# Optimization experiments

Hardware: AMD Instinct MI355X
Metric: run time of the kernel (lower is better)

Reference implementation:

```python
import jax, jax.numpy as jnp
import numpy as np

DIM = 256
HEADS = 8


def _ln(x, g, b, eps=1e-5):
    mu = jnp.mean(x, axis=-1, keepdims=True)
    var = jnp.var(x, axis=-1, keepdims=True)
    return (x - mu) * jax.lax.rsqrt(var + eps) * g + b


def setup_inputs() -> dict:
    key = jax.random.key(0)
    ks = jax.random.split(key, 12)
    d = DIM
    s = lambda fan: 1.0 / np.sqrt(fan)
    return {
        "x": jax.random.normal(ks[0], (1, d, 64, 64), dtype=jnp.float32),
        "ln1_g": jnp.ones((d,), jnp.float32),
        "ln1_b": jnp.zeros((d,), jnp.float32),
        "w_qkv": jax.random.normal(ks[1], (3 * d, d), jnp.float32) * s(d),
        "b_qkv": jnp.zeros((3 * d,), jnp.float32),
        "w_proj": jax.random.normal(ks[2], (d, d), jnp.float32) * s(d),
        "b_proj": jnp.zeros((d,), jnp.float32),
        "ln2_g": jnp.ones((d,), jnp.float32),
        "ln2_b": jnp.zeros((d,), jnp.float32),
        "w_mlp1": jax.random.normal(ks[3], (4 * d, d), jnp.float32) * s(d),
        "b_mlp1": jnp.zeros((4 * d,), jnp.float32),
        "w_mlp2": jax.random.normal(ks[4], (d, 4 * d), jnp.float32) * s(4 * d),
        "b_mlp2": jnp.zeros((d,), jnp.float32),
    }


def reference(x, ln1_g, ln1_b, w_qkv, b_qkv, w_proj, b_proj,
              ln2_g, ln2_b, w_mlp1, b_mlp1, w_mlp2, b_mlp2):
    B, C, H, W = x.shape
    hd = HEADS
    d = C // hd
    scale = d ** (-0.5)
    # work channels-last: [B, H, W, C] -> [B, HW, C]
    xl = jnp.transpose(x, (0, 2, 3, 1)).reshape(B, H * W, C)

    # --- attention branch ---
    xn = _ln(xl, ln1_g, ln1_b)
    qkv = jnp.einsum('bnc,oc->bno', xn, w_qkv) + b_qkv  # [B, N, 3C]
    q, k, v = jnp.split(qkv, 3, axis=-1)
    def heads(t):  # [B,N,C] -> [B,h,N,d]
        return jnp.transpose(t.reshape(B, H * W, hd, d), (0, 2, 1, 3))
    q, k, v = heads(q), heads(k), heads(v)
    attn = jax.nn.softmax(jnp.einsum('bhnd,bhmd->bhnm', q, k) * scale, axis=-1)
    out = jnp.einsum('bhnm,bhmd->bhnd', attn, v)  # [B,h,N,d]
    out = jnp.transpose(out, (0, 2, 1, 3)).reshape(B, H * W, C)
    xl = xl + jnp.einsum('bnc,oc->bno', out, w_proj) + b_proj

    # --- MLP branch ---
    xn = _ln(xl, ln2_g, ln2_b)
    h1 = jax.nn.gelu(jnp.einsum('bnc,oc->bno', xn, w_mlp1) + b_mlp1,
                     approximate=False)
    xl = xl + jnp.einsum('bnf,of->bno', h1, w_mlp2) + b_mlp2

    return jnp.transpose(xl.reshape(B, H, W, C), (0, 3, 1, 2))
```

## Files before the change

kernel.cpp:

```cpp
#include <hip/hip_runtime.h>
#include <hip/hip_bf16.h>

typedef __bf16 bf16_t;
typedef __bf16 bf16x8 __attribute__((ext_vector_type(8)));
typedef __bf16 bf16x4 __attribute__((ext_vector_type(4)));
typedef float  f32x4  __attribute__((ext_vector_type(4)));
typedef unsigned int uint;
typedef uint u32x4 __attribute__((ext_vector_type(4)));

#define MFMA(a,b,c) __builtin_amdgcn_mfma_f32_16x16x32_bf16((a),(b),(c),0,0,0)

__device__ __forceinline__ size_t pidx(int n, int k, int K) {
  return (size_t)(n >> 4) * (K << 4) + ((k >> 3) << 7) + ((n & 15) << 3) + (k & 7);
}

__device__ __forceinline__ uint packbf2(float lo, float hi) {
  unsigned short a = __builtin_bit_cast(unsigned short, (bf16_t)lo);
  unsigned short b = __builtin_bit_cast(unsigned short, (bf16_t)hi);
  return (uint)a | ((uint)b << 16);
}

__global__ __launch_bounds__(256) void prep(const float* __restrict__ w_qkv,
                                            const float* __restrict__ w_proj,
                                            const float* __restrict__ w_mlp1,
                                            const float* __restrict__ w_mlp2,
                                            bf16_t* __restrict__ wq, bf16_t* __restrict__ wp,
                                            bf16_t* __restrict__ w1, bf16_t* __restrict__ w2,
                                            const float* __restrict__ x,
                                            const float* __restrict__ g,
                                            const float* __restrict__ bta,
                                            float* __restrict__ xl,
                                            bf16_t* __restrict__ xn) {
  __shared__ float tile[256][33];
  __shared__ float psum[8][32], psq[8][32], mu_s[32], rs_s[32];
  int b = blockIdx.x;
  if (b < 384) {
    const float* src; bf16_t* dst; int t0, ksh;
    if (b < 96)       { src = w_qkv;  dst = wq; ksh = 5; t0 = b * 256; }
    else if (b < 128) { src = w_proj; dst = wp; ksh = 5; t0 = (b - 96) * 256; }
    else if (b < 256) { src = w_mlp1; dst = w1; ksh = 5; t0 = (b - 128) * 256; }
    else              { src = w_mlp2; dst = w2; ksh = 7; t0 = (b - 256) * 256; }
    int t = t0 + threadIdx.x;
    int n = t >> ksh, kb = t & ((1 << ksh) - 1);
    int K = 8 << ksh;
    const float* p = src + (size_t)n * K + kb * 8;
    float4 a = *(const float4*)p;
    float4 c = *(const float4*)(p + 4);
    bf16x8 o = {(bf16_t)a.x, (bf16_t)a.y, (bf16_t)a.z, (bf16_t)a.w,
                (bf16_t)c.x, (bf16_t)c.y, (bf16_t)c.z, (bf16_t)c.w};
    *(bf16x8*)(dst + (size_t)(n >> 4) * (K << 4) + kb * 128 + ((n & 15) << 3)) = o;
    return;
  }
  int t = threadIdx.x, n0 = (b - 384) * 32;
  int lane32 = t & 31, grp = t >> 5;
#pragma unroll
  for (int it = 0; it < 32; ++it) {
    int c = grp + it * 8;
    tile[c][lane32] = x[(size_t)c * 4096 + n0 + lane32];
  }
  __syncthreads();
  float s = 0.f, sq = 0.f;
#pragma unroll
  for (int ci = 0; ci < 32; ++ci) {
    float v = tile[grp * 32 + ci][lane32];
    s += v; sq += v * v;
  }
  psum[grp][lane32] = s; psq[grp][lane32] = sq;
  __syncthreads();
  if (t < 32) {
    float S = 0.f, Q = 0.f;
#pragma unroll
    for (int p = 0; p < 8; ++p) { S += psum[p][t]; Q += psq[p][t]; }
    float mu = S * (1.0f / 256.0f);
    float var = Q * (1.0f / 256.0f) - mu * mu;
    mu_s[t] = mu; rs_s[t] = rsqrtf(var + 1e-5f);
  }
  __syncthreads();
  {
    float mu = mu_s[lane32], rs = rs_s[lane32];
    int row = n0 + lane32;
    bf16_t* op = xn + (size_t)(row >> 4) * 4096 + ((row & 15) << 3);
#pragma unroll
    for (int cc8 = 0; cc8 < 4; ++cc8) {
      int c0 = grp * 32 + cc8 * 8;
      bf16x8 o;
#pragma unroll
      for (int j = 0; j < 8; ++j) {
        int c = c0 + j;
        o[j] = (bf16_t)((tile[c][lane32] - mu) * rs * g[c] + bta[c]);
      }
      *(bf16x8*)(op + ((c0 >> 3) << 7)) = o;
    }
  }
#pragma unroll
  for (int it = 0; it < 4; ++it) {
    int j = grp + it * 8;
#pragma unroll
    for (int c0 = 0; c0 < 256; c0 += 32)
      xl[(size_t)(n0 + j) * 256 + c0 + lane32] = tile[c0 + lane32][j];
  }
}

template <int K, int EPI, int RPW, int KS = 1>
__global__ __launch_bounds__(256) void gemm_bt(const bf16_t* __restrict__ A,
                                               const bf16_t* __restrict__ W,
                                               const float* __restrict__ bias,
                                               void* __restrict__ outp, int ldn) {
  constexpr int RB = RPW / 16;
  constexpr int KLEN = K / KS;
  int w = threadIdx.x >> 6, lane = threadIdx.x & 63;
  int quad = lane >> 4, idx = lane & 15;
  int row0 = blockIdx.x * (4 * RPW) + w * RPW;
  int col0 = blockIdx.y * 64;
  int kb0 = (KS > 1) ? blockIdx.z * KLEN : 0;
  f32x4 acc[RB][4];
#pragma unroll
  for (int rb = 0; rb < RB; ++rb)
#pragma unroll
    for (int nb = 0; nb < 4; ++nb) acc[rb][nb] = (f32x4){0.f, 0.f, 0.f, 0.f};
  const bf16_t* abase = A + (size_t)(row0 >> 4) * (K << 4) + quad * 128 + idx * 8;
  const bf16_t* wbase = W + (size_t)(col0 >> 4) * (K << 4) + quad * 128 + idx * 8;
#pragma unroll 4
  for (int k0 = kb0; k0 < kb0 + KLEN; k0 += 32) {
    bf16x8 a[RB];
#pragma unroll
    for (int rb = 0; rb < RB; ++rb)
      a[rb] = *(const bf16x8*)(abase + (size_t)rb * (K << 4) + k0 * 16);
#pragma unroll
    for (int nb = 0; nb < 4; ++nb) {
      bf16x8 b = *(const bf16x8*)(wbase + (size_t)nb * (K << 4) + k0 * 16);
#pragma unroll
      for (int rb = 0; rb < RB; ++rb) acc[rb][nb] = MFMA(a[rb], b, acc[rb][nb]);
    }
  }
#pragma unroll
  for (int nb = 0; nb < 4; ++nb) {
    int c = col0 + nb * 16 + idx;
    float bv = (EPI == 4) ? 0.f : bias[c];
#pragma unroll
    for (int rb = 0; rb < RB; ++rb)
#pragma unroll
      for (int r = 0; r < 4; ++r) {
        int rr = row0 + rb * 16 + quad * 4 + r;
        float v = acc[rb][nb][r] + bv;
        if constexpr (EPI == 1) {
          float z = v * (0.7978845608f + 0.0356774081f * v * v);
          float t = __builtin_amdgcn_exp2f(z * 2.885390082f);
          float th = 1.f - 2.f * __builtin_amdgcn_rcpf(t + 1.f);
          v = 0.5f * v * (1.f + th);
          ((bf16_t*)outp)[pidx(rr, c, ldn)] = (bf16_t)v;
        } else if constexpr (EPI == 4) {
          ((float*)outp)[((size_t)blockIdx.z * 4096 + rr) * ldn + c] = v;
        } else {
          bf16_t* qh = (bf16_t*)outp;
          bf16_t* kh = qh + 1048576;
          bf16_t* vp = kh + 1048576;
          if (c < 256) {
            qh[(size_t)(c >> 5) * 131072 + rr * 32 + (c & 31)] = (bf16_t)v;
          } else if (c < 512) {
            kh[(size_t)((c - 256) >> 5) * 131072 + rr * 32 + (c & 31)] = (bf16_t)v;
          } else {
            vp[(size_t)((c - 512) >> 5) * 131072 + (rr >> 5) * 1024 + (c & 31) * 32 + (rr & 31)] = (bf16_t)v;
          }
        }
      }
  }
}

#define SPLIT 4
__device__ __forceinline__ void quad_transpose(const uint p[4][2], bf16x8& lo, bf16x8& hi) {
  auto sA0 = __builtin_amdgcn_permlane32_swap((int)p[0][0], (int)p[1][0], false, false);
  auto sA1 = __builtin_amdgcn_permlane32_swap((int)p[0][1], (int)p[1][1], false, false);
  auto sB0 = __builtin_amdgcn_permlane16_swap(sA0[0], sA0[1], false, false);
  auto sB1 = __builtin_amdgcn_permlane16_swap(sA1[0], sA1[1], false, false);
  u32x4 w0 = {(uint)sB0[0], (uint)sB1[0], (uint)sB0[1], (uint)sB1[1]};
  lo = __builtin_bit_cast(bf16x8, w0);
  auto tA0 = __builtin_amdgcn_permlane32_swap((int)p[2][0], (int)p[3][0], false, false);
  auto tA1 = __builtin_amdgcn_permlane32_swap((int)p[2][1], (int)p[3][1], false, false);
  auto tB0 = __builtin_amdgcn_permlane16_swap(tA0[0], tA0[1], false, false);
  auto tB1 = __builtin_amdgcn_permlane16_swap(tA1[0], tA1[1], false, false);
  u32x4 w1 = {(uint)tB0[0], (uint)tB1[0], (uint)tB0[1], (uint)tB1[1]};
  hi = __builtin_bit_cast(bf16x8, w1);
}

__global__ __launch_bounds__(256, 4) void attn_split(const bf16_t* __restrict__ qkvh,
                                                     uint* __restrict__ o_part,
                                                     float* __restrict__ l_part) {
  int w = threadIdx.x >> 6, lane = threadIdx.x & 63;
  int quad = lane >> 4, idx = lane & 15;
  int h  = blockIdx.x & 7;
  int qt = (blockIdx.x >> 3) & 31;
  int sp = blockIdx.x >> 8;
  int qrow = qt * 128 + w * 32;
  const bf16_t* qh = qkvh + (size_t)h * 131072;
  const bf16_t* kh = qh + 8 * 131072;
  const bf16_t* vp = kh + 8 * 131072;
  const float cs = 0.25503518f;
  bf16x8 qr0 = *(const bf16x8*)(qh + (size_t)(qrow + idx) * 32 + quad * 8);
  bf16x8 qr1 = *(const bf16x8*)(qh + (size_t)(qrow + 16 + idx) * 32 + quad * 8);
  bf16x8 qf0, qf1;
#pragma unroll
  for (int j = 0; j < 8; ++j) {
    qf0[j] = (bf16_t)((float)qr0[j] * cs);
    qf1[j] = (bf16_t)((float)qr1[j] * cs);
  }
  float ls0 = 0.f, ls1 = 0.f;
  f32x4 o00 = {0.f,0.f,0.f,0.f}, o01 = {0.f,0.f,0.f,0.f};
  f32x4 o10 = {0.f,0.f,0.f,0.f}, o11 = {0.f,0.f,0.f,0.f};
  const f32x4 zero = {0.f,0.f,0.f,0.f};
  int kbase = sp * 1024;

  bf16x8 kf[4];
#pragma unroll
  for (int kb = 0; kb < 4; ++kb)
    kf[kb] = *(const bf16x8*)(kh + (size_t)(kbase + kb * 16 + idx) * 32 + quad * 8);

  for (int kt = 0; kt < 16; ++kt) {
    int k0 = kbase + kt * 64;
    int k1 = kbase + ((kt + 1) & 15) * 64;
    const bf16_t* vt = vp + (size_t)(k0 >> 5) * 1024 + quad * 8;
    bf16x8 vv0 = *(const bf16x8*)(vt + idx * 32);
    bf16x8 vv1 = *(const bf16x8*)(vt + (idx + 16) * 32);
    bf16x8 vv2 = *(const bf16x8*)(vt + 1024 + idx * 32);
    bf16x8 vv3 = *(const bf16x8*)(vt + 1024 + (idx + 16) * 32);
    bf16x8 kfn[4];
#pragma unroll
    for (int kb = 0; kb < 4; ++kb)
      kfn[kb] = *(const bf16x8*)(kh + (size_t)(k1 + kb * 16 + idx) * 32 + quad * 8);
    uint p0[4][2], p1[4][2];
#pragma unroll
    for (int kb = 0; kb < 4; ++kb) {
      f32x4 s0 = MFMA(kf[kb], qf0, zero);
      f32x4 s1 = MFMA(kf[kb], qf1, zero);
      float a0 = __builtin_amdgcn_exp2f(s0[0]), a1 = __builtin_amdgcn_exp2f(s0[1]);
      float a2 = __builtin_amdgcn_exp2f(s0[2]), a3 = __builtin_amdgcn_exp2f(s0[3]);
      float b0 = __builtin_amdgcn_exp2f(s1[0]), b1 = __builtin_amdgcn_exp2f(s1[1]);
      float b2 = __builtin_amdgcn_exp2f(s1[2]), b3 = __builtin_amdgcn_exp2f(s1[3]);
      ls0 += (a0 + a1) + (a2 + a3);
      ls1 += (b0 + b1) + (b2 + b3);
      p0[kb][0] = packbf2(a0, a1); p0[kb][1] = packbf2(a2, a3);
      p1[kb][0] = packbf2(b0, b1); p1[kb][1] = packbf2(b2, b3);
    }
    bf16x8 pa0, pa1, pb0, pb1;
    quad_transpose(p0, pa0, pa1);
    quad_transpose(p1, pb0, pb1);
    o00 = MFMA(pa0, vv0, o00);
    o01 = MFMA(pa0, vv1, o01);
    o10 = MFMA(pb0, vv0, o10);
    o11 = MFMA(pb0, vv1, o11);
    o00 = MFMA(pa1, vv2, o00);
    o01 = MFMA(pa1, vv3, o01);
    o10 = MFMA(pb1, vv2, o10);
    o11 = MFMA(pb1, vv3, o11);
#pragma unroll
    for (int kb = 0; kb < 4; ++kb) kf[kb] = kfn[kb];
  }
  ls0 += __shfl_xor(ls0, 16); ls0 += __shfl_xor(ls0, 32);
  ls1 += __shfl_xor(ls1, 16); ls1 += __shfl_xor(ls1, 32);
  if (quad == 0) {
    l_part[((size_t)sp * 8 + h) * 4096 + qrow + idx]      = ls0;
    l_part[((size_t)sp * 8 + h) * 4096 + qrow + 16 + idx] = ls1;
  }
#pragma unroll
  for (int r = 0; r < 4; ++r) {
    int n0 = qrow + quad * 4 + r;
    o_part[(((size_t)sp * 4096 + n0) * 8 + h) * 16 + idx] = packbf2(o00[r], o01[r]);
    int n1 = n0 + 16;
    o_part[(((size_t)sp * 4096 + n1) * 8 + h) * 16 + idx] = packbf2(o10[r], o11[r]);
  }
}

__global__ __launch_bounds__(256) void attn_norm(const uint* __restrict__ o_part,
                                                 const float* __restrict__ l_part,
                                                 bf16_t* __restrict__ attn) {
  int t = blockIdx.x * 256 + threadIdx.x;
  int j0 = (t & 3) * 4;
  int h  = (t >> 2) & 7;
  int n  = t >> 5;
  float l = 0.f;
#pragma unroll
  for (int s = 0; s < SPLIT; ++s) l += l_part[((size_t)s * 8 + h) * 4096 + n];
  float inv = 1.0f / l;
  float alo[4] = {0.f,0.f,0.f,0.f}, ahi[4] = {0.f,0.f,0.f,0.f};
#pragma unroll
  for (int s = 0; s < SPLIT; ++s) {
    const uint* p = o_part + (((size_t)s * 4096 + n) * 8 + h) * 16 + j0;
    uint4 v = *(const uint4*)p;
    uint vv[4] = {v.x, v.y, v.z, v.w};
#pragma unroll
    for (int jj = 0; jj < 4; ++jj) {
      alo[jj] += __builtin_bit_cast(float, vv[jj] << 16);
      ahi[jj] += __builtin_bit_cast(float, vv[jj] & 0xffff0000u);
    }
  }
  bf16x4 lo = {(bf16_t)(alo[0] * inv), (bf16_t)(alo[1] * inv),
               (bf16_t)(alo[2] * inv), (bf16_t)(alo[3] * inv)};
  bf16x4 hi = {(bf16_t)(ahi[0] * inv), (bf16_t)(ahi[1] * inv),
               (bf16_t)(ahi[2] * inv), (bf16_t)(ahi[3] * inv)};
  int k1 = h * 32 + j0;
  int k2 = k1 + 16;
  *(bf16x4*)(attn + (size_t)(n >> 4) * 4096 + ((k1 >> 3) << 7) + ((n & 15) << 3) + (k1 & 7)) = lo;
  *(bf16x4*)(attn + (size_t)(n >> 4) * 4096 + ((k2 >> 3) << 7) + ((n & 15) << 3) + (k2 & 7)) = hi;
}

__global__ __launch_bounds__(256) void combine_ln(const float* __restrict__ pp,
                                                  const float* __restrict__ xl,
                                                  const float* __restrict__ bias,
                                                  const float* __restrict__ g,
                                                  const float* __restrict__ bta,
                                                  float* __restrict__ xl2,
                                                  bf16_t* __restrict__ xn2) {
  int row  = blockIdx.x * 4 + (threadIdx.x >> 6);
  int lane = threadIdx.x & 63;
  size_t ri = (size_t)row * 64 + lane;
  float4 rr = ((const float4*)xl)[ri];
  float4 bb = ((const float4*)bias)[lane];
  float4 v = {rr.x + bb.x, rr.y + bb.y, rr.z + bb.z, rr.w + bb.w};
#pragma unroll
  for (int s = 0; s < 2; ++s) {
    float4 p = ((const float4*)pp)[ri + (size_t)s * 4096 * 64];
    v.x += p.x; v.y += p.y; v.z += p.z; v.w += p.w;
  }
  ((float4*)xl2)[ri] = v;
  float s  = v.x + v.y + v.z + v.w;
  float sq = v.x * v.x + v.y * v.y + v.z * v.z + v.w * v.w;
#pragma unroll
  for (int off = 32; off; off >>= 1) {
    s  += __shfl_xor(s, off);
    sq += __shfl_xor(sq, off);
  }
  float mu  = s * (1.0f / 256.0f);
  float var = sq * (1.0f / 256.0f) - mu * mu;
  float rs  = rsqrtf(var + 1e-5f);
  float4 gg = ((const float4*)g)[lane];
  float4 b2 = ((const float4*)bta)[lane];
  bf16x4 o = {(bf16_t)((v.x - mu) * rs * gg.x + b2.x),
              (bf16_t)((v.y - mu) * rs * gg.y + b2.y),
              (bf16_t)((v.z - mu) * rs * gg.z + b2.z),
              (bf16_t)((v.w - mu) * rs * gg.w + b2.w)};
  int k = lane * 4;
  *(bf16x4*)(xn2 + (size_t)(row >> 4) * 4096 + ((k >> 3) << 7) + ((row & 15) << 3) + (k & 7)) = o;
}

__global__ __launch_bounds__(256) void combine_transpose(const float* __restrict__ mp,
                                                         const float* __restrict__ xl2,
                                                         const float* __restrict__ bias,
                                                         float* __restrict__ dst) {
  __shared__ float tile[32][33];
  int n0 = blockIdx.x * 32, c0 = blockIdx.y * 32;
  int a = threadIdx.x & 31, b = threadIdx.x >> 5;
  float bv = bias[c0 + a];
#pragma unroll
  for (int i = 0; i < 4; ++i) {
    int n = b + i * 8;
    size_t base = (size_t)(n0 + n) * 256 + c0 + a;
    float v = xl2[base] + bv;
#pragma unroll
    for (int s = 0; s < 4; ++s) v += mp[(size_t)s * 1048576 + base];
    tile[a][n] = v;
  }
  __syncthreads();
#pragma unroll
  for (int i = 0; i < 4; ++i) {
    int c = b + i * 8;
    dst[(size_t)(c0 + c) * 4096 + n0 + a] = tile[c][a];
  }
}

extern "C" void kernel_launch(void* const* d_in, const int* in_sizes, int n_in,
                              void* d_out, int out_size, void* d_ws, size_t ws_size,
                              hipStream_t stream) {
  const float* x      = (const float*)d_in[0];
  const float* ln1_g  = (const float*)d_in[1];
  const float* ln1_b  = (const float*)d_in[2];
  const float* w_qkv  = (const float*)d_in[3];
  const float* b_qkv  = (const float*)d_in[4];
  const float* w_proj = (const float*)d_in[5];
  const float* b_proj = (const float*)d_in[6];
  const float* ln2_g  = (const float*)d_in[7];
  const float* ln2_b  = (const float*)d_in[8];
  const float* w_mlp1 = (const float*)d_in[9];
  const float* b_mlp1 = (const float*)d_in[10];
  const float* w_mlp2 = (const float*)d_in[11];
  const float* b_mlp2 = (const float*)d_in[12];

  char* ws = (char*)d_ws;
  bf16_t* qkvh   = (bf16_t*)(ws + 0);
  float*  xl     = (float*)(ws + (6u << 20));
  bf16_t* xn     = (bf16_t*)(ws + (10u << 20));
  uint*   o_part = (uint*)(ws + (12u << 20));
  bf16_t* attn   = (bf16_t*)(ws + (20u << 20));
  float*  pp     = (float*)(ws + (24u << 20));
  float*  xl2    = (float*)(ws + (10u << 20));
  bf16_t* xn2    = (bf16_t*)(ws + (14u << 20));
  bf16_t* h1     = (bf16_t*)(ws + 0);
  float*  mp     = (float*)(ws + (16u << 20));
  bf16_t* wq     = (bf16_t*)(ws + (32u << 20));
  bf16_t* wp     = wq + 196608;
  bf16_t* w1     = wp + 65536;
  bf16_t* w2     = w1 + 262144;
  float*  l_part = (float*)(ws + (34304u << 10));

  prep<<<512, 256, 0, stream>>>(w_qkv, w_proj, w_mlp1, w_mlp2, wq, wp, w1, w2,
                                x, ln1_g, ln1_b, xl, xn);

  gemm_bt<256, 3, 16><<<dim3(64, 12), 256, 0, stream>>>(xn, wq, b_qkv, qkvh, 768);
  attn_split<<<256 * SPLIT, 256, 0, stream>>>(qkvh, o_part, l_part);
  attn_norm<<<512, 256, 0, stream>>>(o_part, l_part, attn);

  gemm_bt<256, 4, 16, 2><<<dim3(64, 4, 2), 256, 0, stream>>>(attn, wp, nullptr, pp, 256);
  combine_ln<<<1024, 256, 0, stream>>>(pp, xl, b_proj, ln2_g, ln2_b, xl2, xn2);

  gemm_bt<256, 1, 16><<<dim3(64, 16), 256, 0, stream>>>(xn2, w1, b_mlp1, h1, 1024);
  gemm_bt<1024, 4, 16, 4><<<dim3(64, 4, 4), 256, 0, stream>>>(h1, w2, nullptr, mp, 256);
  combine_transpose<<<dim3(128, 8), 256, 0, stream>>>(mp, xl2, b_mlp2, (float*)d_out);
}
```

Before: 168.4 us.

## Fuse all stages into one persistent megakernel with atomic grid barriers

Turns each stage into a device function and runs all nine stages inside a single persistent kernel of 1024 blocks, with software grid barriers (atomic counter plus spin) between stages. This removes the per-launch overhead and the idle gaps between nine dependent kernel launches. In exchange, every block now waits at each barrier, the fused kernel needs enough registers and shared memory for the worst stage at occupancy 4, and a memset of the barrier counters is added. The code falls back to separate launches if occupancy is too low, and it relies on all 1024 blocks being resident at once to avoid deadlock.

```diff
diff --git a/kernel.cpp b/kernel.cpp
--- a/kernel.cpp
+++ b/kernel.cpp
@@ -9,6 +9,8 @@
 typedef uint u32x4 __attribute__((ext_vector_type(4)));
 
 #define MFMA(a,b,c) __builtin_amdgcn_mfma_f32_16x16x32_bf16((a),(b),(c),0,0,0)
+#define SPLIT 4
+#define NBLK 1024u
 
 __device__ __forceinline__ size_t pidx(int n, int k, int K) {
   return (size_t)(n >> 4) * (K << 4) + ((k >> 3) << 7) + ((n & 15) << 3) + (k & 7);
@@ -20,20 +22,30 @@
   return (uint)a | ((uint)b << 16);
 }
 
-__global__ __launch_bounds__(256) void prep(const float* __restrict__ w_qkv,
-                                            const float* __restrict__ w_proj,
-                                            const float* __restrict__ w_mlp1,
-                                            const float* __restrict__ w_mlp2,
-                                            bf16_t* __restrict__ wq, bf16_t* __restrict__ wp,
-                                            bf16_t* __restrict__ w1, bf16_t* __restrict__ w2,
-                                            const float* __restrict__ x,
-                                            const float* __restrict__ g,
-                                            const float* __restrict__ bta,
-                                            float* __restrict__ xl,
-                                            bf16_t* __restrict__ xn) {
-  __shared__ float tile[256][33];
-  __shared__ float psum[8][32], psq[8][32], mu_s[32], rs_s[32];
-  int b = blockIdx.x;
+struct PrepSM {
+  float tile[256][33];
+  float psum[8][32], psq[8][32], mu_s[32], rs_s[32];
+};
+struct CtrSM { float tile[32][33]; };
+
+__device__ __forceinline__ void gridbar(uint* bar, int slot) {
+  __threadfence();
+  __syncthreads();
+  if (threadIdx.x == 0) {
+    __hip_atomic_fetch_add(bar + slot * 32, 1u, __ATOMIC_ACQ_REL, __HIP_MEMORY_SCOPE_AGENT);
+    while (__hip_atomic_load(bar + slot * 32, __ATOMIC_ACQUIRE, __HIP_MEMORY_SCOPE_AGENT) < NBLK)
+      __builtin_amdgcn_s_sleep(1);
+  }
+  __syncthreads();
+  __threadfence();
+}
+
+__device__ __forceinline__ void prep_body(int b, char* sm,
+                                          const float* w_qkv, const float* w_proj,
+                                          const float* w_mlp1, const float* w_mlp2,
+                                          bf16_t* wq, bf16_t* wp, bf16_t* w1, bf16_t* w2,
+                                          const float* x, const float* g, const float* bta,
+                                          float* xl, bf16_t* xn) {
   if (b < 384) {
     const float* src; bf16_t* dst; int t0, ksh;
     if (b < 96)       { src = w_qkv;  dst = wq; ksh = 5; t0 = b * 256; }
@@ -51,33 +63,34 @@
     *(bf16x8*)(dst + (size_t)(n >> 4) * (K << 4) + kb * 128 + ((n & 15) << 3)) = o;
     return;
   }
+  PrepSM& S = *(PrepSM*)sm;
   int t = threadIdx.x, n0 = (b - 384) * 32;
   int lane32 = t & 31, grp = t >> 5;
 #pragma unroll
   for (int it = 0; it < 32; ++it) {
     int c = grp + it * 8;
-    tile[c][lane32] = x[(size_t)c * 4096 + n0 + lane32];
+    S.tile[c][lane32] = x[(size_t)c * 4096 + n0 + lane32];
   }
   __syncthreads();
   float s = 0.f, sq = 0.f;
 #pragma unroll
   for (int ci = 0; ci < 32; ++ci) {
-    float v = tile[grp * 32 + ci][lane32];
+    float v = S.tile[grp * 32 + ci][lane32];
     s += v; sq += v * v;
   }
-  psum[grp][lane32] = s; psq[grp][lane32] = sq;
+  S.psum[grp][lane32] = s; S.psq[grp][lane32] = sq;
   __syncthreads();
   if (t < 32) {
-    float S = 0.f, Q = 0.f;
-#pragma unroll
-    for (int p = 0; p < 8; ++p) { S += psum[p][t]; Q += psq[p][t]; }
-    float mu = S * (1.0f / 256.0f);
+    float Su = 0.f, Q = 0.f;
+#pragma unroll
+    for (int p = 0; p < 8; ++p) { Su += S.psum[p][t]; Q += S.psq[p][t]; }
+    float mu = Su * (1.0f / 256.0f);
     float var = Q * (1.0f / 256.0f) - mu * mu;
-    mu_s[t] = mu; rs_s[t] = rsqrtf(var + 1e-5f);
+    S.mu_s[t] = mu; S.rs_s[t] = rsqrtf(var + 1e-5f);
   }
   __syncthreads();
   {
-    float mu = mu_s[lane32], rs = rs_s[lane32];
+    float mu = S.mu_s[lane32], rs = S.rs_s[lane32];
     int row = n0 + lane32;
     bf16_t* op = xn + (size_t)(row >> 4) * 4096 + ((row & 15) << 3);
 #pragma unroll
@@ -87,7 +100,7 @@
 #pragma unroll
       for (int j = 0; j < 8; ++j) {
         int c = c0 + j;
-        o[j] = (bf16_t)((tile[c][lane32] - mu) * rs * g[c] + bta[c]);
+        o[j] = (bf16_t)((S.tile[c][lane32] - mu) * rs * g[c] + bta[c]);
       }
       *(bf16x8*)(op + ((c0 >> 3) << 7)) = o;
     }
@@ -97,22 +110,21 @@
     int j = grp + it * 8;
 #pragma unroll
     for (int c0 = 0; c0 < 256; c0 += 32)
-      xl[(size_t)(n0 + j) * 256 + c0 + lane32] = tile[c0 + lane32][j];
-  }
-}
-
-template <int K, int EPI, int RPW, int KS = 1>
-__global__ __launch_bounds__(256) void gemm_bt(const bf16_t* __restrict__ A,
-                                               const bf16_t* __restrict__ W,
-                                               const float* __restrict__ bias,
-                                               void* __restrict__ outp, int ldn) {
+      xl[(size_t)(n0 + j) * 256 + c0 + lane32] = S.tile[c0 + lane32][j];
+  }
+}
+
+template <int K, int EPI, int RPW, int KS>
+__device__ __forceinline__ void gemm_body(int bx, int by, int bz,
+                                          const bf16_t* A, const bf16_t* W,
+                                          const float* bias, void* outp, int ldn) {
   constexpr int RB = RPW / 16;
   constexpr int KLEN = K / KS;
   int w = threadIdx.x >> 6, lane = threadIdx.x & 63;
   int quad = lane >> 4, idx = lane & 15;
-  int row0 = blockIdx.x * (4 * RPW) + w * RPW;
-  int col0 = blockIdx.y * 64;
-  int kb0 = (KS > 1) ? blockIdx.z * KLEN : 0;
+  int row0 = bx * (4 * RPW) + w * RPW;
+  int col0 = by * 64;
+  int kb0 = (KS > 1) ? bz * KLEN : 0;
   f32x4 acc[RB][4];
 #pragma unroll
   for (int rb = 0; rb < RB; ++rb)
@@ -150,7 +162,7 @@
           v = 0.5f * v * (1.f + th);
           ((bf16_t*)outp)[pidx(rr, c, ldn)] = (bf16_t)v;
         } else if constexpr (EPI == 4) {
-          ((float*)outp)[((size_t)blockIdx.z * 4096 + rr) * ldn + c] = v;
+          ((float*)outp)[((size_t)bz * 4096 + rr) * ldn + c] = v;
         } else {
           bf16_t* qh = (bf16_t*)outp;
           bf16_t* kh = qh + 1048576;
@@ -167,7 +179,6 @@
   }
 }
 
-#define SPLIT 4
 __device__ __forceinline__ void quad_transpose(const uint p[4][2], bf16x8& lo, bf16x8& hi) {
   auto sA0 = __builtin_amdgcn_permlane32_swap((int)p[0][0], (int)p[1][0], false, false);
   auto sA1 = __builtin_amdgcn_permlane32_swap((int)p[0][1], (int)p[1][1], false, false);
@@ -183,14 +194,13 @@
   hi = __builtin_bit_cast(bf16x8, w1);
 }
 
-__global__ __launch_bounds__(256, 4) void attn_split(const bf16_t* __restrict__ qkvh,
-                                                     uint* __restrict__ o_part,
-                                                     float* __restrict__ l_part) {
+__device__ __forceinline__ void attn_body(int bid, const bf16_t* qkvh,
+                                          uint* o_part, float* l_part) {
   int w = threadIdx.x >> 6, lane = threadIdx.x & 63;
   int quad = lane >> 4, idx = lane & 15;
-  int h  = blockIdx.x & 7;
-  int qt = (blockIdx.x >> 3) & 31;
-  int sp = blockIdx.x >> 8;
+  int h  = bid & 7;
+  int qt = (bid >> 3) & 31;
+  int sp = bid >> 8;
   int qrow = qt * 128 + w * 32;
   const bf16_t* qh = qkvh + (size_t)h * 131072;
   const bf16_t* kh = qh + 8 * 131072;
@@ -270,10 +280,9 @@
   }
 }
 
-__global__ __launch_bounds__(256) void attn_norm(const uint* __restrict__ o_part,
-                                                 const float* __restrict__ l_part,
-                                                 bf16_t* __restrict__ attn) {
-  int t = blockIdx.x * 256 + threadIdx.x;
+__device__ __forceinline__ void attn_norm_body(int bid, const uint* o_part,
+                                               const float* l_part, bf16_t* attn) {
+  int t = bid * 256 + threadIdx.x;
   int j0 = (t & 3) * 4;
   int h  = (t >> 2) & 7;
   int n  = t >> 5;
@@ -303,14 +312,10 @@
   *(bf16x4*)(attn + (size_t)(n >> 4) * 4096 + ((k2 >> 3) << 7) + ((n & 15) << 3) + (k2 & 7)) = hi;
 }
 
-__global__ __launch_bounds__(256) void combine_ln(const float* __restrict__ pp,
-                                                  const float* __restrict__ xl,
-                                                  const float* __restrict__ bias,
-                                                  const float* __restrict__ g,
-                                                  const float* __restrict__ bta,
-                                                  float* __restrict__ xl2,
-                                                  bf16_t* __restrict__ xn2) {
-  int row  = blockIdx.x * 4 + (threadIdx.x >> 6);
+__device__ __forceinline__ void combine_ln_body(int bid, const float* pp, const float* xl,
+                                                const float* bias, const float* g,
+                                                const float* bta, float* xl2, bf16_t* xn2) {
+  int row  = bid * 4 + (threadIdx.x >> 6);
   int lane = threadIdx.x & 63;
   size_t ri = (size_t)row * 64 + lane;
   float4 rr = ((const float4*)xl)[ri];
@@ -342,12 +347,11 @@
   *(bf16x4*)(xn2 + (size_t)(row >> 4) * 4096 + ((k >> 3) << 7) + ((row & 15) << 3) + (k & 7)) = o;
 }
 
-__global__ __launch_bounds__(256) void combine_transpose(const float* __restrict__ mp,
-                                                         const float* __restrict__ xl2,
-                                                         const float* __restrict__ bias,
-                                                         float* __restrict__ dst) {
-  __shared__ float tile[32][33];
-  int n0 = blockIdx.x * 32, c0 = blockIdx.y * 32;
+__device__ __forceinline__ void combine_transpose_body(int bx, int by, char* sm,
+                                                       const float* mp, const float* xl2,
+                                                       const float* bias, float* dst) {
+  CtrSM& S = *(CtrSM*)sm;
+  int n0 = bx * 32, c0 = by * 32;
   int a = threadIdx.x & 31, b = threadIdx.x >> 5;
   float bv = bias[c0 + a];
 #pragma unroll
@@ -357,14 +361,96 @@
     float v = xl2[base] + bv;
 #pragma unroll
     for (int s = 0; s < 4; ++s) v += mp[(size_t)s * 1048576 + base];
-    tile[a][n] = v;
+    S.tile[a][n] = v;
   }
   __syncthreads();
 #pragma unroll
   for (int i = 0; i < 4; ++i) {
     int c = b + i * 8;
-    dst[(size_t)(c0 + c) * 4096 + n0 + a] = tile[c][a];
-  }
+    dst[(size_t)(c0 + c) * 4096 + n0 + a] = S.tile[c][a];
+  }
+}
+
+__global__ __launch_bounds__(256, 4) void mega(const float* x,
+                                               const float* ln1_g, const float* ln1_b,
+                                               const float* w_qkv, const float* b_qkv,
+                                               const float* w_proj, const float* b_proj,
+                                               const float* ln2_g, const float* ln2_b,
+                                               const float* w_mlp1, const float* b_mlp1,
+                                               const float* w_mlp2, const float* b_mlp2,
+                                               float* out, char* ws) {
+  __shared__ __align__(16) char sm[sizeof(PrepSM)];
+  int bid = blockIdx.x;
+
+  bf16_t* qkvh   = (bf16_t*)(ws + 0);
+  float*  xl     = (float*)(ws + (6u << 20));
+  bf16_t* xn     = (bf16_t*)(ws + (10u << 20));
+  uint*   o_part = (uint*)(ws + (12u << 20));
+  bf16_t* attn   = (bf16_t*)(ws + (20u << 20));
+  float*  pp     = (float*)(ws + (24u << 20));
+  float*  xl2    = (float*)(ws + (10u << 20));
+  bf16_t* xn2    = (bf16_t*)(ws + (14u << 20));
+  bf16_t* h1     = (bf16_t*)(ws + 0);
+  float*  mp     = (float*)(ws + (16u << 20));
+  bf16_t* wq     = (bf16_t*)(ws + (32u << 20));
+  bf16_t* wp     = wq + 196608;
+  bf16_t* w1     = wp + 65536;
+  bf16_t* w2     = w1 + 262144;
+  float*  l_part = (float*)(ws + (34304u << 10));
+  uint*   bar    = (uint*)(ws + (34u << 20));
+
+  if (bid < 512)
+    prep_body(bid, sm, w_qkv, w_proj, w_mlp1, w_mlp2, wq, wp, w1, w2,
+              x, ln1_g, ln1_b, xl, xn);
+  gridbar(bar, 0);
+  if (bid < 768)
+    gemm_body<256, 3, 16, 1>(bid & 63, bid >> 6, 0, xn, wq, b_qkv, qkvh, 768);
+  gridbar(bar, 1);
+  attn_body(bid, qkvh, o_part, l_part);
+  gridbar(bar, 2);
+  if (bid < 512)
+    attn_norm_body(bid, o_part, l_part, attn);
+  gridbar(bar, 3);
+  if (bid < 512)
+    gemm_body<256, 4, 16, 2>(bid & 63, (bid >> 6) & 3, bid >> 8, attn, wp, nullptr, pp, 256);
+  gridbar(bar, 4);
+  combine_ln_body(bid, pp, xl, b_proj, ln2_g, ln2_b, xl2, xn2);
+  gridbar(bar, 5);
+  gemm_body<256, 1, 16, 1>(bid & 63, bid >> 6, 0, xn2, w1, b_mlp1, h1, 1024);
+  gridbar(bar, 6);
+  gemm_body<1024, 4, 16, 4>(bid & 63, (bid >> 6) & 3, bid >> 8, h1, w2, nullptr, mp, 256);
+  gridbar(bar, 7);
+  combine_transpose_body(bid & 127, bid >> 7, sm, mp, xl2, b_mlp2, out);
+}
+
+__global__ __launch_bounds__(256) void prep_k(const float* w_qkv, const float* w_proj,
+                                              const float* w_mlp1, const float* w_mlp2,
+                                              bf16_t* wq, bf16_t* wp, bf16_t* w1, bf16_t* w2,
+                                              const float* x, const float* g,
+                                              const float* bta, float* xl, bf16_t* xn) {
+  __shared__ __align__(16) char sm[sizeof(PrepSM)];
+  prep_body(blockIdx.x, sm, w_qkv, w_proj, w_mlp1, w_mlp2, wq, wp, w1, w2, x, g, bta, xl, xn);
+}
+template <int K, int EPI, int RPW, int KS = 1>
+__global__ __launch_bounds__(256) void gemm_k(const bf16_t* A, const bf16_t* W,
+                                              const float* bias, void* outp, int ldn) {
+  gemm_body<K, EPI, RPW, KS>(blockIdx.x, blockIdx.y, blockIdx.z, A, W, bias, outp, ldn);
+}
+__global__ __launch_bounds__(256, 4) void attn_k(const bf16_t* qkvh, uint* o_part, float* l_part) {
+  attn_body(blockIdx.x, qkvh, o_part, l_part);
+}
+__global__ __launch_bounds__(256) void attn_norm_k(const uint* o_part, const float* l_part, bf16_t* attn) {
+  attn_norm_body(blockIdx.x, o_part, l_part, attn);
+}
+__global__ __launch_bounds__(256) void combine_ln_k(const float* pp, const float* xl,
+                                                    const float* bias, const float* g,
+                                                    const float* bta, float* xl2, bf16_t* xn2) {
+  combine_ln_body(blockIdx.x, pp, xl, bias, g, bta, xl2, xn2);
+}
+__global__ __launch_bounds__(256) void combine_transpose_k(const float* mp, const float* xl2,
+                                                           const float* bias, float* dst) {
+  __shared__ __align__(16) char sm[sizeof(CtrSM)];
+  combine_transpose_body(blockIdx.x, blockIdx.y, sm, mp, xl2, bias, dst);
 }
 
 extern "C" void kernel_launch(void* const* d_in, const int* in_sizes, int n_in,
@@ -383,8 +469,9 @@
   const float* b_mlp1 = (const float*)d_in[10];
   const float* w_mlp2 = (const float*)d_in[11];
   const float* b_mlp2 = (const float*)d_in[12];
-
+  float* out = (float*)d_out;
   char* ws = (char*)d_ws;
+
   bf16_t* qkvh   = (bf16_t*)(ws + 0);
   float*  xl     = (float*)(ws + (6u << 20));
   bf16_t* xn     = (bf16_t*)(ws + (10u << 20));
@@ -400,18 +487,31 @@
   bf16_t* w1     = wp + 65536;
   bf16_t* w2     = w1 + 262144;
   float*  l_part = (float*)(ws + (34304u << 10));
-
-  prep<<<512, 256, 0, stream>>>(w_qkv, w_proj, w_mlp1, w_mlp2, wq, wp, w1, w2,
-                                x, ln1_g, ln1_b, xl, xn);
-
-  gemm_bt<256, 3, 16><<<dim3(64, 12), 256, 0, stream>>>(xn, wq, b_qkv, qkvh, 768);
-  attn_split<<<256 * SPLIT, 256, 0, stream>>>(qkvh, o_part, l_part);
-  attn_norm<<<512, 256, 0, stream>>>(o_part, l_part, attn);
-
-  gemm_bt<256, 4, 16, 2><<<dim3(64, 4, 2), 256, 0, stream>>>(attn, wp, nullptr, pp, 256);
-  combine_ln<<<1024, 256, 0, stream>>>(pp, xl, b_proj, ln2_g, ln2_b, xl2, xn2);
-
-  gemm_bt<256, 1, 16><<<dim3(64, 16), 256, 0, stream>>>(xn2, w1, b_mlp1, h1, 1024);
-  gemm_bt<1024, 4, 16, 4><<<dim3(64, 4, 4), 256, 0, stream>>>(h1, w2, nullptr, mp, 256);
-  combine_transpose<<<dim3(128, 8), 256, 0, stream>>>(mp, xl2, b_mlp2, (float*)d_out);
-}
+  uint*   bar    = (uint*)(ws + (34u << 20));
+
+  static int mega_ok = -1;
+  if (mega_ok < 0) {
+    int nb = 0;
+    hipError_t e = hipOccupancyMaxActiveBlocksPerMultiprocessor(&nb, mega, 256, 0);
+    mega_ok = (e == hipSuccess && nb >= 4) ? 1 : 0;
+  }
+
+  if (mega_ok) {
+    hipMemsetAsync(bar, 0, 4096, stream);
+    mega<<<NBLK, 256, 0, stream>>>(x, ln1_g, ln1_b, w_qkv, b_qkv, w_proj, b_proj,
+                                   ln2_g, ln2_b, w_mlp1, b_mlp1, w_mlp2, b_mlp2,
+                                   out, ws);
+    return;
+  }
+
+  prep_k<<<512, 256, 0, stream>>>(w_qkv, w_proj, w_mlp1, w_mlp2, wq, wp, w1, w2,
+                                  x, ln1_g, ln1_b, xl, xn);
+  gemm_k<256, 3, 16><<<dim3(64, 12), 256, 0, stream>>>(xn, wq, b_qkv, qkvh, 768);
+  attn_k<<<256 * SPLIT, 256, 0, stream>>>(qkvh, o_part, l_part);
+  attn_norm_k<<<512, 256, 0, stream>>>(o_part, l_part, attn);
+  gemm_k<256, 4, 16, 2><<<dim3(64, 4, 2), 256, 0, stream>>>(attn, wp, nullptr, pp, 256);
+  combine_ln_k<<<1024, 256, 0, stream>>>(pp, xl, b_proj, ln2_g, ln2_b, xl2, xn2);
+  gemm_k<256, 1, 16><<<dim3(64, 16), 256, 0, stream>>>(xn2, w1, b_mlp1, h1, 1024);
+  gemm_k<1024, 4, 16, 4><<<dim3(64, 4, 4), 256, 0, stream>>>(h1, w2, nullptr, mp, 256);
+  combine_transpose_k<<<dim3(128, 8), 256, 0, stream>>>(mp, xl2, b_mlp2, (float*)d_out);
+}
```

Result: no change. 169.3 us (+0.5%).

## Halve query rows per wave in split attention to double occupancy

Applied to the files above, without the earlier changes.

Each attention wave now handles 16 query rows instead of 32, so twice as many blocks are launched and launch bounds ask for 8 blocks per CU. The software prefetch of the next K tile is dropped and K is loaded inline. The aim is to cut register pressure and raise occupancy so more waves hide latency. In exchange, each K/V tile is reused across fewer query rows, which doubles K/V load traffic, and K loads are no longer overlapped with the previous tile's compute.

```diff
diff --git a/kernel.cpp b/kernel.cpp
--- a/kernel.cpp
+++ b/kernel.cpp
@@ -9,6 +9,7 @@
 typedef uint u32x4 __attribute__((ext_vector_type(4)));
 
 #define MFMA(a,b,c) __builtin_amdgcn_mfma_f32_16x16x32_bf16((a),(b),(c),0,0,0)
+#define SPLIT 4
 
 __device__ __forceinline__ size_t pidx(int n, int k, int K) {
   return (size_t)(n >> 4) * (K << 4) + ((k >> 3) << 7) + ((n & 15) << 3) + (k & 7);
@@ -167,7 +168,6 @@
   }
 }
 
-#define SPLIT 4
 __device__ __forceinline__ void quad_transpose(const uint p[4][2], bf16x8& lo, bf16x8& hi) {
   auto sA0 = __builtin_amdgcn_permlane32_swap((int)p[0][0], (int)p[1][0], false, false);
   auto sA1 = __builtin_amdgcn_permlane32_swap((int)p[0][1], (int)p[1][1], false, false);
@@ -183,90 +183,59 @@
   hi = __builtin_bit_cast(bf16x8, w1);
 }
 
-__global__ __launch_bounds__(256, 4) void attn_split(const bf16_t* __restrict__ qkvh,
+__global__ __launch_bounds__(256, 8) void attn_split(const bf16_t* __restrict__ qkvh,
                                                      uint* __restrict__ o_part,
                                                      float* __restrict__ l_part) {
   int w = threadIdx.x >> 6, lane = threadIdx.x & 63;
   int quad = lane >> 4, idx = lane & 15;
   int h  = blockIdx.x & 7;
-  int qt = (blockIdx.x >> 3) & 31;
-  int sp = blockIdx.x >> 8;
-  int qrow = qt * 128 + w * 32;
+  int qt = (blockIdx.x >> 3) & 63;
+  int sp = blockIdx.x >> 9;
+  int qrow = qt * 64 + w * 16;
   const bf16_t* qh = qkvh + (size_t)h * 131072;
   const bf16_t* kh = qh + 8 * 131072;
   const bf16_t* vp = kh + 8 * 131072;
   const float cs = 0.25503518f;
   bf16x8 qr0 = *(const bf16x8*)(qh + (size_t)(qrow + idx) * 32 + quad * 8);
-  bf16x8 qr1 = *(const bf16x8*)(qh + (size_t)(qrow + 16 + idx) * 32 + quad * 8);
-  bf16x8 qf0, qf1;
-#pragma unroll
-  for (int j = 0; j < 8; ++j) {
-    qf0[j] = (bf16_t)((float)qr0[j] * cs);
-    qf1[j] = (bf16_t)((float)qr1[j] * cs);
-  }
-  float ls0 = 0.f, ls1 = 0.f;
+  bf16x8 qf0;
+#pragma unroll
+  for (int j = 0; j < 8; ++j) qf0[j] = (bf16_t)((float)qr0[j] * cs);
+  float ls0 = 0.f;
   f32x4 o00 = {0.f,0.f,0.f,0.f}, o01 = {0.f,0.f,0.f,0.f};
-  f32x4 o10 = {0.f,0.f,0.f,0.f}, o11 = {0.f,0.f,0.f,0.f};
   const f32x4 zero = {0.f,0.f,0.f,0.f};
   int kbase = sp * 1024;
 
-  bf16x8 kf[4];
-#pragma unroll
-  for (int kb = 0; kb < 4; ++kb)
-    kf[kb] = *(const bf16x8*)(kh + (size_t)(kbase + kb * 16 + idx) * 32 + quad * 8);
-
   for (int kt = 0; kt < 16; ++kt) {
     int k0 = kbase + kt * 64;
-    int k1 = kbase + ((kt + 1) & 15) * 64;
     const bf16_t* vt = vp + (size_t)(k0 >> 5) * 1024 + quad * 8;
     bf16x8 vv0 = *(const bf16x8*)(vt + idx * 32);
     bf16x8 vv1 = *(const bf16x8*)(vt + (idx + 16) * 32);
     bf16x8 vv2 = *(const bf16x8*)(vt + 1024 + idx * 32);
     bf16x8 vv3 = *(const bf16x8*)(vt + 1024 + (idx + 16) * 32);
-    bf16x8 kfn[4];
-#pragma unroll
-    for (int kb = 0; kb < 4; ++kb)
-      kfn[kb] = *(const bf16x8*)(kh + (size_t)(k1 + kb * 16 + idx) * 32 + quad * 8);
-    uint p0[4][2], p1[4][2];
+    uint p0[4][2];
 #pragma unroll
     for (int kb = 0; kb < 4; ++kb) {
-      f32x4 s0 = MFMA(kf[kb], qf0, zero);
-      f32x4 s1 = MFMA(kf[kb], qf1, zero);
+      bf16x8 kf = *(const bf16x8*)(kh + (size_t)(k0 + kb * 16 + idx) * 32 + quad * 8);
+      f32x4 s0 = MFMA(kf, qf0, zero);
       float a0 = __builtin_amdgcn_exp2f(s0[0]), a1 = __builtin_amdgcn_exp2f(s0[1]);
       float a2 = __builtin_amdgcn_exp2f(s0[2]), a3 = __builtin_amdgcn_exp2f(s0[3]);
-      float b0 = __builtin_amdgcn_exp2f(s1[0]), b1 = __builtin_amdgcn_exp2f(s1[1]);
-      float b2 = __builtin_amdgcn_exp2f(s1[2]), b3 = __builtin_amdgcn_exp2f(s1[3]);
       ls0 += (a0 + a1) + (a2 + a3);
-      ls1 += (b0 + b1) + (b2 + b3);
       p0[kb][0] = packbf2(a0, a1); p0[kb][1] = packbf2(a2, a3);
-      p1[kb][0] = packbf2(b0, b1); p1[kb][1] = packbf2(b2, b3);
     }
-    bf16x8 pa0, pa1, pb0, pb1;
+    bf16x8 pa0, pa1;
     quad_transpose(p0, pa0, pa1);
-    quad_transpose(p1, pb0, pb1);
     o00 = MFMA(pa0, vv0, o00);
     o01 = MFMA(pa0, vv1, o01);
-    o10 = MFMA(pb0, vv0, o10);
-    o11 = MFMA(pb0, vv1, o11);
     o00 = MFMA(pa1, vv2, o00);
     o01 = MFMA(pa1, vv3, o01);
-    o10 = MFMA(pb1, vv2, o10);
-    o11 = MFMA(pb1, vv3, o11);
-#pragma unroll
-    for (int kb = 0; kb < 4; ++kb) kf[kb] = kfn[kb];
   }
   ls0 += __shfl_xor(ls0, 16); ls0 += __shfl_xor(ls0, 32);
-  ls1 += __shfl_xor(ls1, 16); ls1 += __shfl_xor(ls1, 32);
-  if (quad == 0) {
-    l_part[((size_t)sp * 8 + h) * 4096 + qrow + idx]      = ls0;
-    l_part[((size_t)sp * 8 + h) * 4096 + qrow + 16 + idx] = ls1;
-  }
+  if (quad == 0)
+    l_part[((size_t)sp * 8 + h) * 4096 + qrow + idx] = ls0;
 #pragma unroll
   for (int r = 0; r < 4; ++r) {
     int n0 = qrow + quad * 4 + r;
     o_part[(((size_t)sp * 4096 + n0) * 8 + h) * 16 + idx] = packbf2(o00[r], o01[r]);
-    int n1 = n0 + 16;
-    o_part[(((size_t)sp * 4096 + n1) * 8 + h) * 16 + idx] = packbf2(o10[r], o11[r]);
   }
 }
 
@@ -405,7 +374,7 @@
                                 x, ln1_g, ln1_b, xl, xn);
 
   gemm_bt<256, 3, 16><<<dim3(64, 12), 256, 0, stream>>>(xn, wq, b_qkv, qkvh, 768);
-  attn_split<<<256 * SPLIT, 256, 0, stream>>>(qkvh, o_part, l_part);
+  attn_split<<<512 * SPLIT, 256, 0, stream>>>(qkvh, o_part, l_part);
   attn_norm<<<512, 256, 0, stream>>>(o_part, l_part, attn);
 
   gemm_bt<256, 4, 16, 2><<<dim3(64, 4, 2), 256, 0, stream>>>(attn, wp, nullptr, pp, 256);
```

Measured after the change: 193.2 us. 14.8% more time.

## Fold reduction epilogues into producer kernels via last-arrival atomic counters

Applied to the files above, without the earlier changes.

Removes the separate attn_norm, combine_ln and combine_transpose launches. The last block of each group to finish, detected with an atomic ticket counter, performs the split-K or split-KV reduction plus the following elementwise work. This saves three kernel launches and their inter-kernel gaps. In exchange it adds a memset, threadfences and atomics, and the tail work now runs serially in a few last blocks, which may leave the GPU underutilized at the end of each kernel.

```diff
diff --git a/kernel.cpp b/kernel.cpp
--- a/kernel.cpp
+++ b/kernel.cpp
@@ -9,6 +9,7 @@
 typedef uint u32x4 __attribute__((ext_vector_type(4)));
 
 #define MFMA(a,b,c) __builtin_amdgcn_mfma_f32_16x16x32_bf16((a),(b),(c),0,0,0)
+#define SPLIT 4
 
 __device__ __forceinline__ size_t pidx(int n, int k, int K) {
   return (size_t)(n >> 4) * (K << 4) + ((k >> 3) << 7) + ((n & 15) << 3) + (k & 7);
@@ -18,6 +19,20 @@
   unsigned short a = __builtin_bit_cast(unsigned short, (bf16_t)lo);
   unsigned short b = __builtin_bit_cast(unsigned short, (bf16_t)hi);
   return (uint)a | ((uint)b << 16);
+}
+
+__device__ __forceinline__ bool last_arrival(uint* tk, int grp, uint members) {
+  __syncthreads();
+  __threadfence();
+  __shared__ uint oldv;
+  __syncthreads();
+  if (threadIdx.x == 0)
+    oldv = __hip_atomic_fetch_add(tk + grp, 1u, __ATOMIC_ACQ_REL,
+                                  __HIP_MEMORY_SCOPE_AGENT);
+  __syncthreads();
+  bool last = (oldv == members - 1);
+  if (last) __threadfence();
+  return last;
 }
 
 __global__ __launch_bounds__(256) void prep(const float* __restrict__ w_qkv,
@@ -101,11 +116,18 @@
   }
 }
 
-template <int K, int EPI, int RPW, int KS = 1>
+template <int K, int EPI, int RPW, int KS = 1, int FOLD = 0>
 __global__ __launch_bounds__(256) void gemm_bt(const bf16_t* __restrict__ A,
                                                const bf16_t* __restrict__ W,
                                                const float* __restrict__ bias,
-                                               void* __restrict__ outp, int ldn) {
+                                               void* __restrict__ outp, int ldn,
+                                               uint* __restrict__ tk,
+                                               const float* __restrict__ f0,
+                                               const float* __restrict__ f1,
+                                               const float* __restrict__ f2,
+                                               const float* __restrict__ f3,
+                                               float* __restrict__ f4,
+                                               void* __restrict__ f5) {
   constexpr int RB = RPW / 16;
   constexpr int KLEN = K / KS;
   int w = threadIdx.x >> 6, lane = threadIdx.x & 63;
@@ -165,9 +187,82 @@
         }
       }
   }
-}
-
-#define SPLIT 4
+
+  if constexpr (FOLD == 1) {
+    if (last_arrival(tk, blockIdx.x, 8)) {
+      int t = threadIdx.x;
+      int ln = t & 63;
+      const float* pp = (const float*)outp;
+#pragma unroll 2
+      for (int rr = 0; rr < 16; ++rr) {
+        int row = blockIdx.x * 64 + rr * 4 + (t >> 6);
+        size_t ri = (size_t)row * 64 + ln;
+        float4 r4 = ((const float4*)f0)[ri];
+        float4 bb = ((const float4*)f1)[ln];
+        float4 v = {r4.x + bb.x, r4.y + bb.y, r4.z + bb.z, r4.w + bb.w};
+#pragma unroll
+        for (int s = 0; s < 2; ++s) {
+          float4 p = ((const float4*)pp)[ri + (size_t)s * 4096 * 64];
+          v.x += p.x; v.y += p.y; v.z += p.z; v.w += p.w;
+        }
+        ((float4*)f4)[ri] = v;
+        float s  = v.x + v.y + v.z + v.w;
+        float sq = v.x * v.x + v.y * v.y + v.z * v.z + v.w * v.w;
+#pragma unroll
+        for (int off = 32; off; off >>= 1) {
+          s  += __shfl_xor(s, off);
+          sq += __shfl_xor(sq, off);
+        }
+        float mu  = s * (1.0f / 256.0f);
+        float var = sq * (1.0f / 256.0f) - mu * mu;
+        float rs  = rsqrtf(var + 1e-5f);
+        float4 gg = ((const float4*)f2)[ln];
+        float4 b2 = ((const float4*)f3)[ln];
+        bf16x4 o = {(bf16_t)((v.x - mu) * rs * gg.x + b2.x),
+                    (bf16_t)((v.y - mu) * rs * gg.y + b2.y),
+                    (bf16_t)((v.z - mu) * rs * gg.z + b2.z),
+                    (bf16_t)((v.w - mu) * rs * gg.w + b2.w)};
+        int k = ln * 4;
+        *(bf16x4*)((bf16_t*)f5 + (size_t)(row >> 4) * 4096 + ((k >> 3) << 7) +
+                   ((row & 15) << 3) + (k & 7)) = o;
+      }
+    }
+  }
+
+  if constexpr (FOLD == 2) {
+    if (last_arrival(tk, blockIdx.x, 16)) {
+      __shared__ float tile[32][33];
+      int t = threadIdx.x;
+      int a = t & 31, b = t >> 5;
+      const float* mp = (const float*)outp;
+      for (int sub = 0; sub < 16; ++sub) {
+        int n0 = (blockIdx.x * 2 + (sub >> 3)) * 32;
+        int c0 = (sub & 7) * 32;
+        float bv = f1[c0 + a];
+        float vals[4];
+#pragma unroll
+        for (int i = 0; i < 4; ++i) {
+          int n = b + i * 8;
+          size_t base = (size_t)(n0 + n) * 256 + c0 + a;
+          float v = f0[base] + bv;
+#pragma unroll
+          for (int s = 0; s < 4; ++s) v += mp[(size_t)s * 1048576 + base];
+          vals[i] = v;
+        }
+        if (sub) __syncthreads();
+#pragma unroll
+        for (int i = 0; i < 4; ++i) tile[a][b + i * 8] = vals[i];
+        __syncthreads();
+#pragma unroll
+        for (int i = 0; i < 4; ++i) {
+          int c = b + i * 8;
+          f4[(size_t)(c0 + c) * 4096 + n0 + a] = tile[c][a];
+        }
+      }
+    }
+  }
+}
+
 __device__ __forceinline__ void quad_transpose(const uint p[4][2], bf16x8& lo, bf16x8& hi) {
   auto sA0 = __builtin_amdgcn_permlane32_swap((int)p[0][0], (int)p[1][0], false, false);
   auto sA1 = __builtin_amdgcn_permlane32_swap((int)p[0][1], (int)p[1][1], false, false);
@@ -185,7 +280,9 @@
 
 __global__ __launch_bounds__(256, 4) void attn_split(const bf16_t* __restrict__ qkvh,
                                                      uint* __restrict__ o_part,
-                                                     float* __restrict__ l_part) {
+                                                     float* __restrict__ l_part,
+                                                     uint* __restrict__ tk,
+                                                     bf16_t* __restrict__ attn) {
   int w = threadIdx.x >> 6, lane = threadIdx.x & 63;
   int quad = lane >> 4, idx = lane & 15;
   int h  = blockIdx.x & 7;
@@ -268,102 +365,39 @@
     int n1 = n0 + 16;
     o_part[(((size_t)sp * 4096 + n1) * 8 + h) * 16 + idx] = packbf2(o10[r], o11[r]);
   }
-}
-
-__global__ __launch_bounds__(256) void attn_norm(const uint* __restrict__ o_part,
-                                                 const float* __restrict__ l_part,
-                                                 bf16_t* __restrict__ attn) {
-  int t = blockIdx.x * 256 + threadIdx.x;
-  int j0 = (t & 3) * 4;
-  int h  = (t >> 2) & 7;
-  int n  = t >> 5;
-  float l = 0.f;
-#pragma unroll
-  for (int s = 0; s < SPLIT; ++s) l += l_part[((size_t)s * 8 + h) * 4096 + n];
-  float inv = 1.0f / l;
-  float alo[4] = {0.f,0.f,0.f,0.f}, ahi[4] = {0.f,0.f,0.f,0.f};
-#pragma unroll
-  for (int s = 0; s < SPLIT; ++s) {
-    const uint* p = o_part + (((size_t)s * 4096 + n) * 8 + h) * 16 + j0;
-    uint4 v = *(const uint4*)p;
-    uint vv[4] = {v.x, v.y, v.z, v.w};
-#pragma unroll
-    for (int jj = 0; jj < 4; ++jj) {
-      alo[jj] += __builtin_bit_cast(float, vv[jj] << 16);
-      ahi[jj] += __builtin_bit_cast(float, vv[jj] & 0xffff0000u);
-    }
-  }
-  bf16x4 lo = {(bf16_t)(alo[0] * inv), (bf16_t)(alo[1] * inv),
-               (bf16_t)(alo[2] * inv), (bf16_t)(alo[3] * inv)};
-  bf16x4 hi = {(bf16_t)(ahi[0] * inv), (bf16_t)(ahi[1] * inv),
-               (bf16_t)(ahi[2] * inv), (bf16_t)(ahi[3] * inv)};
-  int k1 = h * 32 + j0;
-  int k2 = k1 + 16;
-  *(bf16x4*)(attn + (size_t)(n >> 4) * 4096 + ((k1 >> 3) << 7) + ((n & 15) << 3) + (k1 & 7)) = lo;
-  *(bf16x4*)(attn + (size_t)(n >> 4) * 4096 + ((k2 >> 3) << 7) + ((n & 15) << 3) + (k2 & 7)) = hi;
-}
-
-__global__ __launch_bounds__(256) void combine_ln(const float* __restrict__ pp,
-                                                  const float* __restrict__ xl,
-                                                  const float* __restrict__ bias,
-                                                  const float* __restrict__ g,
-                                                  const float* __restrict__ bta,
-                                                  float* __restrict__ xl2,
-                                                  bf16_t* __restrict__ xn2) {
-  int row  = blockIdx.x * 4 + (threadIdx.x >> 6);
-  int lane = threadIdx.x & 63;
-  size_t ri = (size_t)row * 64 + lane;
-  float4 rr = ((const float4*)xl)[ri];
-  float4 bb = ((const float4*)bias)[lane];
-  float4 v = {rr.x + bb.x, rr.y + bb.y, rr.z + bb.z, rr.w + bb.w};
-#pragma unroll
-  for (int s = 0; s < 2; ++s) {
-    float4 p = ((const float4*)pp)[ri + (size_t)s * 4096 * 64];
-    v.x += p.x; v.y += p.y; v.z += p.z; v.w += p.w;
-  }
-  ((float4*)xl2)[ri] = v;
-  float s  = v.x + v.y + v.z + v.w;
-  float sq = v.x * v.x + v.y * v.y + v.z * v.z + v.w * v.w;
-#pragma unroll
-  for (int off = 32; off; off >>= 1) {
-    s  += __shfl_xor(s, off);
-    sq += __shfl_xor(sq, off);
-  }
-  float mu  = s * (1.0f / 256.0f);
-  float var = sq * (1.0f / 256.0f) - mu * mu;
-  float rs  = rsqrtf(var + 1e-5f);
-  float4 gg = ((const float4*)g)[lane];
-  float4 b2 = ((const float4*)bta)[lane];
-  bf16x4 o = {(bf16_t)((v.x - mu) * rs * gg.x + b2.x),
-              (bf16_t)((v.y - mu) * rs * gg.y + b2.y),
-              (bf16_t)((v.z - mu) * rs * gg.z + b2.z),
-              (bf16_t)((v.w - mu) * rs * gg.w + b2.w)};
-  int k = lane * 4;
-  *(bf16x4*)(xn2 + (size_t)(row >> 4) * 4096 + ((k >> 3) << 7) + ((row & 15) << 3) + (k & 7)) = o;
-}
-
-__global__ __launch_bounds__(256) void combine_transpose(const float* __restrict__ mp,
-                                                         const float* __restrict__ xl2,
-                                                         const float* __restrict__ bias,
-                                                         float* __restrict__ dst) {
-  __shared__ float tile[32][33];
-  int n0 = blockIdx.x * 32, c0 = blockIdx.y * 32;
-  int a = threadIdx.x & 31, b = threadIdx.x >> 5;
-  float bv = bias[c0 + a];
-#pragma unroll
-  for (int i = 0; i < 4; ++i) {
-    int n = b + i * 8;
-    size_t base = (size_t)(n0 + n) * 256 + c0 + a;
-    float v = xl2[base] + bv;
-#pragma unroll
-    for (int s = 0; s < 4; ++s) v += mp[(size_t)s * 1048576 + base];
-    tile[a][n] = v;
-  }
-  __syncthreads();
-#pragma unroll
-  for (int i = 0; i < 4; ++i) {
-    int c = b + i * 8;
-    dst[(size_t)(c0 + c) * 4096 + n0 + a] = tile[c][a];
+
+  if (last_arrival(tk, qt * 8 + h, 4)) {
+    int t = threadIdx.x;
+#pragma unroll
+    for (int it = 0; it < 2; ++it) {
+      int u = t + it * 256;
+      int n = qt * 128 + (u >> 2);
+      int j0 = (u & 3) * 4;
+      float l = 0.f;
+#pragma unroll
+      for (int s = 0; s < SPLIT; ++s) l += l_part[((size_t)s * 8 + h) * 4096 + n];
+      float inv = 1.0f / l;
+      float alo[4] = {0.f,0.f,0.f,0.f}, ahi[4] = {0.f,0.f,0.f,0.f};
+#pragma unroll
+      for (int s = 0; s < SPLIT; ++s) {
+        const uint* p = o_part + (((size_t)s * 4096 + n) * 8 + h) * 16 + j0;
+        uint4 v = *(const uint4*)p;
+        uint vv[4] = {v.x, v.y, v.z, v.w};
+#pragma unroll
+        for (int jj = 0; jj < 4; ++jj) {
+          alo[jj] += __builtin_bit_cast(float, vv[jj] << 16);
+          ahi[jj] += __builtin_bit_cast(float, vv[jj] & 0xffff0000u);
+        }
+      }
+      bf16x4 lo = {(bf16_t)(alo[0] * inv), (bf16_t)(alo[1] * inv),
+                   (bf16_t)(alo[2] * inv), (bf16_t)(alo[3] * inv)};
+      bf16x4 hi = {(bf16_t)(ahi[0] * inv), (bf16_t)(ahi[1] * inv),
+                   (bf16_t)(ahi[2] * inv), (bf16_t)(ahi[3] * inv)};
+      int k1 = h * 32 + j0;
+      int k2 = k1 + 16;
+      *(bf16x4*)(attn + (size_t)(n >> 4) * 4096 + ((k1 >> 3) << 7) + ((n & 15) << 3) + (k1 & 7)) = lo;
+      *(bf16x4*)(attn + (size_t)(n >> 4) * 4096 + ((k2 >> 3) << 7) + ((n & 15) << 3) + (k2 & 7)) = hi;
+    }
   }
 }
 
@@ -400,18 +434,22 @@
   bf16_t* w1     = wp + 65536;
   bf16_t* w2     = w1 + 262144;
   float*  l_part = (float*)(ws + (34304u << 10));
+  uint*   tk     = (uint*)(ws + (35u << 20));
+
+  hipMemsetAsync(tk, 0, 4096, stream);
 
   prep<<<512, 256, 0, stream>>>(w_qkv, w_proj, w_mlp1, w_mlp2, wq, wp, w1, w2,
                                 x, ln1_g, ln1_b, xl, xn);
 
-  gemm_bt<256, 3, 16><<<dim3(64, 12), 256, 0, stream>>>(xn, wq, b_qkv, qkvh, 768);
-  attn_split<<<256 * SPLIT, 256, 0, stream>>>(qkvh, o_part, l_part);
-  attn_norm<<<512, 256, 0, stream>>>(o_part, l_part, attn);
-
-  gemm_bt<256, 4, 16, 2><<<dim3(64, 4, 2), 256, 0, stream>>>(attn, wp, nullptr, pp, 256);
-  combine_ln<<<1024, 256, 0, stream>>>(pp, xl, b_proj, ln2_g, ln2_b, xl2, xn2);
-
-  gemm_bt<256, 1, 16><<<dim3(64, 16), 256, 0, stream>>>(xn2, w1, b_mlp1, h1, 1024);
-  gemm_bt<1024, 4, 16, 4><<<dim3(64, 4, 4), 256, 0, stream>>>(h1, w2, nullptr, mp, 256);
-  combine_transpose<<<dim3(128, 8), 256, 0, stream>>>(mp, xl2, b_mlp2, (float*)d_out);
-}
+  gemm_bt<256, 3, 16><<<dim3(64, 12), 256, 0, stream>>>(
+      xn, wq, b_qkv, qkvh, 768, nullptr, nullptr, nullptr, nullptr, nullptr, nullptr, nullptr);
+  attn_split<<<256 * SPLIT, 256, 0, stream>>>(qkvh, o_part, l_part, tk, attn);
+
+  gemm_bt<256, 4, 16, 2, 1><<<dim3(64, 4, 2), 256, 0, stream>>>(
+      attn, wp, nullptr, pp, 256, tk + 256, xl, b_proj, ln2_g, ln2_b, xl2, xn2);
+
+  gemm_bt<256, 1, 16><<<dim3(64, 16), 256, 0, stream>>>(
+      xn2, w1, b_mlp1, h1, 1024, nullptr, nullptr, nullptr, nullptr, nullptr, nullptr, nullptr);
+  gemm_bt<1024, 4, 16, 4, 2><<<dim3(64, 4, 4), 256, 0, stream>>>(
+      h1, w2, nullptr, mp, 256, tk + 512, xl2, b_mlp2, nullptr, nullptr, (float*)d_out, nullptr);
+}
```

After: 502.9 us. +198.7%, slower.
